# Kernel tuning notes

Hardware: AMD Instinct MI355X
Metric: run time of the kernel (lower is better)

## Reference

```python
import jax, jax.numpy as jnp
import numpy as np

H = 1024
V = 50257
S = 8192


def setup_inputs() -> dict:
    key = jax.random.key(0)
    ks = jax.random.split(key, 13)
    s = 0.02  # param init scale
    return {
        "input": jax.random.randint(ks[0], (1,), 0, V),
        "hidden": jax.random.normal(ks[1], (1, 1, H), jnp.float32),
        "encoder_outputs": jax.random.normal(ks[2], (S, H), jnp.float32),
        "embedding": jax.random.normal(ks[3], (V, H), jnp.float32) * s,
        "attn_w": jax.random.normal(ks[4], (1, 2 * H), jnp.float32) * s,
        "attn_b": jnp.zeros((1,), jnp.float32),
        "comb_w": jax.random.normal(ks[5], (H, 2 * H), jnp.float32) * s,
        "comb_b": jnp.zeros((H,), jnp.float32),
        "w_ih": jax.random.normal(ks[6], (3 * H, H), jnp.float32) * s,
        "w_hh": jax.random.normal(ks[7], (3 * H, H), jnp.float32) * s,
        "b_ih": jnp.zeros((3 * H,), jnp.float32),
        "b_hh": jnp.zeros((3 * H,), jnp.float32),
        "out_w": jax.random.normal(ks[8], (V, H), jnp.float32) * s,
        "out_b": jnp.zeros((V,), jnp.float32),
    }


def reference(input, hidden, encoder_outputs, embedding, attn_w, attn_b,
              comb_w, comb_b, w_ih, w_hh, b_ih, b_hh, out_w, out_b):
    # embedded = embedding(input).view(1,1,-1); dropout in eval mode = identity
    emb = embedding[input[0]]            # [H]
    h0 = hidden[0, 0]                    # [H]
    # Original loop computes the SAME score attn(cat(emb, hidden)) for every
    # timestep -> softmax over a constant vector (uniform weights). Compute the
    # scalar once and broadcast (same math, one GEMV instead of S launches).
    score = jnp.concatenate([emb, h0]) @ attn_w[0] + attn_b[0]   # scalar
    seq_len = encoder_outputs.shape[0]
    attn_weights = jax.nn.softmax(jnp.broadcast_to(score, (seq_len,)))  # [S]
    attn_applied = attn_weights @ encoder_outputs                # [H]
    combined = jnp.concatenate([emb, attn_applied]) @ comb_w.T + comb_b  # [H]
    x = jax.nn.relu(combined)
    # Single GRU step (torch nn.GRU gate math)
    gi = w_ih @ x + b_ih                 # [3H]
    gh = w_hh @ h0 + b_hh                # [3H]
    i_r, i_z, i_n = jnp.split(gi, 3)
    h_r, h_z, h_n = jnp.split(gh, 3)
    r = jax.nn.sigmoid(i_r + h_r)
    z = jax.nn.sigmoid(i_z + h_z)
    n = jnp.tanh(i_n + r * h_n)
    h_new = (1.0 - z) * n + z * h0       # [H]
    logits = h_new @ out_w.T + out_b     # [V]
    output = jax.nn.log_softmax(logits)[None, :]   # [1, V]
    return output, h_new[None, None, :], attn_weights[None, :]
```

## Files before the change

kernel.cpp:

```cpp
#include <hip/hip_runtime.h>
#include <math.h>

#define HN 1024
#define VN 50257
#define SN 8192

#define WS_PARTIAL 0
#define WS_AA      262144
#define WS_X       263168
#define WS_G       264192
#define WS_LOGITS  271360
#define WS_EXPD    321618

__device__ __forceinline__ float wred(float v) {
#pragma unroll
  for (int m = 32; m; m >>= 1) v += __shfl_xor(v, m);
  return v;
}

__device__ __forceinline__ float dot4(float4 a, float4 b) {
  return a.x * b.x + a.y * b.y + a.z * b.z + a.w * b.w;
}

__global__ void k1_front(const float* __restrict__ enc,
                         const float* __restrict__ w_hh,
                         const float* __restrict__ hidden,
                         float* __restrict__ ws, float* __restrict__ out_attn) {
  const int blk = blockIdx.x, t = threadIdx.x;
  if (blk < 256) {
    const float4* e4 = (const float4*)enc + (size_t)blk * 32 * 256;
    float4 acc = make_float4(0.f, 0.f, 0.f, 0.f);
#pragma unroll 8
    for (int r = 0; r < 32; ++r) {
      float4 v = e4[r * 256 + t];
      acc.x += v.x; acc.y += v.y; acc.z += v.z; acc.w += v.w;
    }
    ((float4*)(ws + WS_PARTIAL))[blk * 256 + t] = acc;
  } else if (blk < 512) {
    const int w = t >> 6, l = t & 63;
    const int wgid = (blk - 256) * 4 + w;
    const float4* h4 = (const float4*)hidden;
    float4 hv0 = h4[l], hv1 = h4[64 + l], hv2 = h4[128 + l], hv3 = h4[192 + l];
#pragma unroll
    for (int k = 0; k < 3; ++k) {
      const int r = wgid + k * 1024;
      const float4* m4 = (const float4*)w_hh + (size_t)r * 256;
      float acc = dot4(m4[l], hv0) + dot4(m4[64 + l], hv1) +
                  dot4(m4[128 + l], hv2) + dot4(m4[192 + l], hv3);
      acc = wred(acc);
      if (l == 0) ws[WS_G + 3072 + r] = acc;
    }
  } else {
#pragma unroll
    for (int j = 0; j < 32; ++j) out_attn[t + j * 256] = 1.f / 8192.f;
  }
}

__global__ void k2_reduce(float* __restrict__ ws) {
  const int c = blockIdx.x * 256 + threadIdx.x;
  const float* p = ws + WS_PARTIAL;
  float s = 0.f;
#pragma unroll 8
  for (int rc = 0; rc < 256; ++rc) s += p[rc * 1024 + c];
  ws[WS_AA + c] = s * (1.f / 8192.f);
}

__global__ void k3_combined(const int* __restrict__ token,
                            const float* __restrict__ embedding,
                            const float* __restrict__ comb_w,
                            const float* __restrict__ comb_b,
                            float* __restrict__ ws) {
  const int w = threadIdx.x >> 6, l = threadIdx.x & 63;
  const int i = blockIdx.x * 4 + w;
  const int tok = token[0];
  const float4* emb4 = (const float4*)embedding + (size_t)tok * 256;
  const float4* aa4 = (const float4*)(ws + WS_AA);
  const float4* cw4 = (const float4*)comb_w + (size_t)i * 512;
  float acc = 0.f;
#pragma unroll
  for (int k = 0; k < 8; ++k) {
    float4 wv = cw4[k * 64 + l];
    float4 xv = (k < 4) ? emb4[k * 64 + l] : aa4[(k - 4) * 64 + l];
    acc += dot4(wv, xv);
  }
  acc = wred(acc);
  if (l == 0) {
    float c = acc + comb_b[i];
    ws[WS_X + i] = fmaxf(c, 0.f);
  }
}

__global__ void k4_gates(const float* __restrict__ w_ih, float* __restrict__ ws) {
  const int w = threadIdx.x >> 6, l = threadIdx.x & 63;
  const int r = blockIdx.x * 4 + w;
  const float4* m4 = (const float4*)w_ih + (size_t)r * 256;
  const float4* x4 = (const float4*)(ws + WS_X);
  float acc = 0.f;
#pragma unroll
  for (int k = 0; k < 4; ++k) acc += dot4(m4[k * 64 + l], x4[k * 64 + l]);
  acc = wred(acc);
  if (l == 0) ws[WS_G + r] = acc;
}

__global__ void k5_logits(const float* __restrict__ b_ih, const float* __restrict__ b_hh,
                          const float* __restrict__ hidden,
                          const float* __restrict__ out_w, const float* __restrict__ out_b,
                          float* __restrict__ ws, float* __restrict__ d_out) {
  const int blk = blockIdx.x, t = threadIdx.x;
  const int w = t >> 6, l = t & 63;
  __shared__ float4 hs4[256];
  __shared__ double sd[4];
  float* hsf = (float*)hs4;
  const float* g = ws + WS_G;
#pragma unroll
  for (int j = 0; j < 4; ++j) {
    const int i = t + j * 256;
    float ir = g[i] + b_ih[i];
    float iz = g[i + 1024] + b_ih[i + 1024];
    float inn = g[i + 2048] + b_ih[i + 2048];
    float hr = g[3072 + i] + b_hh[i];
    float hz = g[3072 + i + 1024] + b_hh[i + 1024];
    float hn = g[3072 + i + 2048] + b_hh[i + 2048];
    float rg = 1.f / (1.f + expf(-(ir + hr)));
    float zg = 1.f / (1.f + expf(-(iz + hz)));
    float ng = tanhf(inn + rg * hn);
    float h = (1.f - zg) * ng + zg * hidden[i];
    hsf[i] = h;
    if (blk == 0) d_out[VN + i] = h;
  }
  __syncthreads();

  float4 h0_ = hs4[l], h1_ = hs4[64 + l], h2_ = hs4[128 + l], h3_ = hs4[192 + l];
  const float4* ow4 = (const float4*)out_w;
  double eacc = 0.0;
  const int gw = blk * 4 + w;
  for (int v = gw; v < VN; v += 4096) {
    const float4* row = ow4 + (size_t)v * 256;
    float acc = dot4(row[l], h0_) + dot4(row[64 + l], h1_) +
                dot4(row[128 + l], h2_) + dot4(row[192 + l], h3_);
    acc = wred(acc);
    if (l == 0) {
      float lg = acc + out_b[v];
      ws[WS_LOGITS + v] = lg;
      eacc += (double)expf(lg);
    }
  }
  if (l == 0) sd[w] = eacc;
  __syncthreads();
  if (t == 0) ((double*)(ws + WS_EXPD))[blk] = sd[0] + sd[1] + sd[2] + sd[3];
}

__global__ void k6_final(const float* __restrict__ ws, float* __restrict__ d_out) {
  __shared__ double sd[256];
  const int t = threadIdx.x;
  const double* ed = (const double*)(ws + WS_EXPD);
  sd[t] = ed[t] + ed[t + 256] + ed[t + 512] + ed[t + 768];
  __syncthreads();
  for (int s = 128; s; s >>= 1) {
    if (t < s) sd[t] += sd[t + s];
    __syncthreads();
  }
  const float logZ = (float)log(sd[0]);
  const int v = blockIdx.x * 256 + t;
  if (v < VN) d_out[v] = ws[WS_LOGITS + v] - logZ;
}

extern "C" void kernel_launch(void* const* d_in, const int* in_sizes, int n_in,
                              void* d_out, int out_size, void* d_ws, size_t ws_size,
                              hipStream_t stream) {
  const int* token = (const int*)d_in[0];
  const float* hidden = (const float*)d_in[1];
  const float* enc = (const float*)d_in[2];
  const float* embedding = (const float*)d_in[3];
  const float* comb_w = (const float*)d_in[6];
  const float* comb_b = (const float*)d_in[7];
  const float* w_ih = (const float*)d_in[8];
  const float* w_hh = (const float*)d_in[9];
  const float* b_ih = (const float*)d_in[10];
  const float* b_hh = (const float*)d_in[11];
  const float* out_w = (const float*)d_in[12];
  const float* out_b = (const float*)d_in[13];
  float* out = (float*)d_out;
  float* ws = (float*)d_ws;

  k1_front<<<513, 256, 0, stream>>>(enc, w_hh, hidden, ws, out + VN + HN);
  k2_reduce<<<4, 256, 0, stream>>>(ws);
  k3_combined<<<256, 256, 0, stream>>>(token, embedding, comb_w, comb_b, ws);
  k4_gates<<<768, 256, 0, stream>>>(w_ih, ws);
  k5_logits<<<1024, 256, 0, stream>>>(b_ih, b_hh, hidden, out_w, out_b, ws, out);
  k6_final<<<197, 256, 0, stream>>>(ws, out);
}
```

Before: 72.22 us.

## Rebalance front reduction, split GRU update out, and double rows per warp in logits

The encoder column-sum kernel now uses 1024-thread blocks that each split 32 rows across 4 groups and combine the partials in LDS. The attention-weight fill moves into those blocks, and the w_hh GEMV gets 64 blocks of 16 warps. The second reduction spreads over 32 blocks with an LDS combine instead of 4 blocks of long serial loops. The GRU gate computation moves out of every logits block into a single-block kernel, so 1024 blocks no longer recompute h_new redundantly. The logits kernel uses 2048 blocks with two output rows per warp per iteration to raise memory-level parallelism, at the cost of one extra launch.

```diff
diff --git a/kernel.cpp b/kernel.cpp
--- a/kernel.cpp
+++ b/kernel.cpp
@@ -9,6 +9,7 @@
 #define WS_AA      262144
 #define WS_X       263168
 #define WS_G       264192
+#define WS_HNEW    270336
 #define WS_LOGITS  271360
 #define WS_EXPD    321618
 
@@ -22,47 +23,63 @@
   return a.x * b.x + a.y * b.y + a.z * b.z + a.w * b.w;
 }
 
-__global__ void k1_front(const float* __restrict__ enc,
-                         const float* __restrict__ w_hh,
-                         const float* __restrict__ hidden,
-                         float* __restrict__ ws, float* __restrict__ out_attn) {
+__global__ __launch_bounds__(1024) void k1_front(
+    const float* __restrict__ enc, const float* __restrict__ w_hh,
+    const float* __restrict__ hidden, float* __restrict__ ws,
+    float* __restrict__ out_attn) {
   const int blk = blockIdx.x, t = threadIdx.x;
   if (blk < 256) {
-    const float4* e4 = (const float4*)enc + (size_t)blk * 32 * 256;
+    __shared__ float4 lds[1024];
+    const int g = t >> 8, c4 = t & 255;
+    const float4* e4 = (const float4*)enc + ((size_t)blk * 32 + g * 8) * 256 + c4;
     float4 acc = make_float4(0.f, 0.f, 0.f, 0.f);
-#pragma unroll 8
-    for (int r = 0; r < 32; ++r) {
-      float4 v = e4[r * 256 + t];
+#pragma unroll
+    for (int r = 0; r < 8; ++r) {
+      float4 v = e4[r * 256];
       acc.x += v.x; acc.y += v.y; acc.z += v.z; acc.w += v.w;
     }
-    ((float4*)(ws + WS_PARTIAL))[blk * 256 + t] = acc;
-  } else if (blk < 512) {
-    const int w = t >> 6, l = t & 63;
-    const int wgid = (blk - 256) * 4 + w;
+    lds[t] = acc;
+    __syncthreads();
+    if (t < 256) {
+      float4 a = lds[t], b = lds[t + 256], c = lds[t + 512], d = lds[t + 768];
+      float4 s = make_float4(a.x + b.x + c.x + d.x, a.y + b.y + c.y + d.y,
+                             a.z + b.z + c.z + d.z, a.w + b.w + c.w + d.w);
+      ((float4*)(ws + WS_PARTIAL))[blk * 256 + t] = s;
+    }
+    if (t < 32) out_attn[blk * 32 + t] = 1.f / 8192.f;
+  } else {
+    const int wg = (blk - 256) * 16 + (t >> 6);
+    const int l = t & 63;
     const float4* h4 = (const float4*)hidden;
     float4 hv0 = h4[l], hv1 = h4[64 + l], hv2 = h4[128 + l], hv3 = h4[192 + l];
 #pragma unroll
     for (int k = 0; k < 3; ++k) {
-      const int r = wgid + k * 1024;
+      const int r = wg + k * 1024;
       const float4* m4 = (const float4*)w_hh + (size_t)r * 256;
       float acc = dot4(m4[l], hv0) + dot4(m4[64 + l], hv1) +
                   dot4(m4[128 + l], hv2) + dot4(m4[192 + l], hv3);
       acc = wred(acc);
       if (l == 0) ws[WS_G + 3072 + r] = acc;
     }
-  } else {
-#pragma unroll
-    for (int j = 0; j < 32; ++j) out_attn[t + j * 256] = 1.f / 8192.f;
   }
 }
 
 __global__ void k2_reduce(float* __restrict__ ws) {
-  const int c = blockIdx.x * 256 + threadIdx.x;
+  __shared__ float lds[256];
+  const int t = threadIdx.x, b = blockIdx.x;
+  const int c = b * 32 + (t & 31), rg = t >> 5;
   const float* p = ws + WS_PARTIAL;
   float s = 0.f;
 #pragma unroll 8
-  for (int rc = 0; rc < 256; ++rc) s += p[rc * 1024 + c];
-  ws[WS_AA + c] = s * (1.f / 8192.f);
+  for (int j = 0; j < 32; ++j) s += p[(rg * 32 + j) * 1024 + c];
+  lds[t] = s;
+  __syncthreads();
+  if (t < 32) {
+    float a = 0.f;
+#pragma unroll
+    for (int j = 0; j < 8; ++j) a += lds[j * 32 + t];
+    ws[WS_AA + b * 32 + t] = a * (1.f / 8192.f);
+  }
 }
 
 __global__ void k3_combined(const int* __restrict__ token,
@@ -102,15 +119,10 @@
   if (l == 0) ws[WS_G + r] = acc;
 }
 
-__global__ void k5_logits(const float* __restrict__ b_ih, const float* __restrict__ b_hh,
-                          const float* __restrict__ hidden,
-                          const float* __restrict__ out_w, const float* __restrict__ out_b,
-                          float* __restrict__ ws, float* __restrict__ d_out) {
-  const int blk = blockIdx.x, t = threadIdx.x;
-  const int w = t >> 6, l = t & 63;
-  __shared__ float4 hs4[256];
-  __shared__ double sd[4];
-  float* hsf = (float*)hs4;
+__global__ void k4b_hnew(const float* __restrict__ b_ih, const float* __restrict__ b_hh,
+                         const float* __restrict__ hidden, float* __restrict__ ws,
+                         float* __restrict__ d_out) {
+  const int t = threadIdx.x;
   const float* g = ws + WS_G;
 #pragma unroll
   for (int j = 0; j < 4; ++j) {
@@ -125,26 +137,43 @@
     float zg = 1.f / (1.f + expf(-(iz + hz)));
     float ng = tanhf(inn + rg * hn);
     float h = (1.f - zg) * ng + zg * hidden[i];
-    hsf[i] = h;
-    if (blk == 0) d_out[VN + i] = h;
-  }
-  __syncthreads();
-
-  float4 h0_ = hs4[l], h1_ = hs4[64 + l], h2_ = hs4[128 + l], h3_ = hs4[192 + l];
+    ws[WS_HNEW + i] = h;
+    d_out[VN + i] = h;
+  }
+}
+
+__global__ void k5_logits(const float* __restrict__ out_w, const float* __restrict__ out_b,
+                          float* __restrict__ ws) {
+  const int blk = blockIdx.x, t = threadIdx.x;
+  const int w = t >> 6, l = t & 63;
+  const int gw = blk * 4 + w;
+  const float4* h4p = (const float4*)(ws + WS_HNEW);
+  float4 h0_ = h4p[l], h1_ = h4p[64 + l], h2_ = h4p[128 + l], h3_ = h4p[192 + l];
   const float4* ow4 = (const float4*)out_w;
   double eacc = 0.0;
-  const int gw = blk * 4 + w;
-  for (int v = gw; v < VN; v += 4096) {
-    const float4* row = ow4 + (size_t)v * 256;
-    float acc = dot4(row[l], h0_) + dot4(row[64 + l], h1_) +
-                dot4(row[128 + l], h2_) + dot4(row[192 + l], h3_);
-    acc = wred(acc);
+  for (int v = gw; v < VN; v += 16384) {
+    const int v2 = v + 8192;
+    const bool ok2 = (v2 < VN);
+    const float4* r0 = ow4 + (size_t)v * 256;
+    const float4* r1 = ow4 + (size_t)(ok2 ? v2 : v) * 256;
+    float acc0 = dot4(r0[l], h0_) + dot4(r0[64 + l], h1_) +
+                 dot4(r0[128 + l], h2_) + dot4(r0[192 + l], h3_);
+    float acc1 = dot4(r1[l], h0_) + dot4(r1[64 + l], h1_) +
+                 dot4(r1[128 + l], h2_) + dot4(r1[192 + l], h3_);
+    acc0 = wred(acc0);
+    acc1 = wred(acc1);
     if (l == 0) {
-      float lg = acc + out_b[v];
-      ws[WS_LOGITS + v] = lg;
-      eacc += (double)expf(lg);
-    }
-  }
+      float lg0 = acc0 + out_b[v];
+      ws[WS_LOGITS + v] = lg0;
+      eacc += (double)expf(lg0);
+      if (ok2) {
+        float lg1 = acc1 + out_b[v2];
+        ws[WS_LOGITS + v2] = lg1;
+        eacc += (double)expf(lg1);
+      }
+    }
+  }
+  __shared__ double sd[4];
   if (l == 0) sd[w] = eacc;
   __syncthreads();
   if (t == 0) ((double*)(ws + WS_EXPD))[blk] = sd[0] + sd[1] + sd[2] + sd[3];
@@ -154,7 +183,10 @@
   __shared__ double sd[256];
   const int t = threadIdx.x;
   const double* ed = (const double*)(ws + WS_EXPD);
-  sd[t] = ed[t] + ed[t + 256] + ed[t + 512] + ed[t + 768];
+  double a = 0.0;
+#pragma unroll
+  for (int j = 0; j < 8; ++j) a += ed[t + j * 256];
+  sd[t] = a;
   __syncthreads();
   for (int s = 128; s; s >>= 1) {
     if (t < s) sd[t] += sd[t + s];
@@ -183,10 +215,11 @@
   float* out = (float*)d_out;
   float* ws = (float*)d_ws;
 
-  k1_front<<<513, 256, 0, stream>>>(enc, w_hh, hidden, ws, out + VN + HN);
-  k2_reduce<<<4, 256, 0, stream>>>(ws);
+  k1_front<<<320, 1024, 0, stream>>>(enc, w_hh, hidden, ws, out + VN + HN);
+  k2_reduce<<<32, 256, 0, stream>>>(ws);
   k3_combined<<<256, 256, 0, stream>>>(token, embedding, comb_w, comb_b, ws);
   k4_gates<<<768, 256, 0, stream>>>(w_ih, ws);
-  k5_logits<<<1024, 256, 0, stream>>>(b_ih, b_hh, hidden, out_w, out_b, ws, out);
+  k4b_hnew<<<1, 256, 0, stream>>>(b_ih, b_hh, hidden, ws, out);
+  k5_logits<<<2048, 256, 0, stream>>>(out_w, out_b, ws);
   k6_final<<<197, 256, 0, stream>>>(ws, out);
 }
```

Result: faster. 63.76 us (-11.7%).
